# Kernel optimization log

Hardware: AMD Instinct MI355X
Metric: run time of the kernel (lower is better)

Reference implementation:

```python
import jax, jax.numpy as jnp
import numpy as np

DIM = 128        # per-head dim == model width in this module
Q_HEADS = 16
KV_HEADS = 4
WINDOW = 512
BATCH = 4
SEQ = 2048


def setup_inputs() -> dict:
    key = jax.random.key(0)
    k1, k2, k3 = jax.random.split(key, 3)
    x = jax.random.normal(k1, (BATCH, SEQ, DIM), dtype=jnp.float32)
    # fused qkv weight, stored (in, out) so forward is x @ W_qkv
    W_qkv = jax.random.normal(k2, (DIM, (Q_HEADS + 2 * KV_HEADS) * DIM), dtype=jnp.float32) * (DIM ** -0.5)
    W_proj = jax.random.normal(k3, (Q_HEADS * DIM, DIM), dtype=jnp.float32) * ((Q_HEADS * DIM) ** -0.5)
    return {"x": x, "W_qkv": W_qkv, "W_proj": W_proj}


def _gqa_forward(x, W_qkv, W_proj):
    b, s, d = x.shape
    qkv = x @ W_qkv                                    # [b, s, (Hq+2Hkv)*d]
    qkv = qkv.reshape(b, s, Q_HEADS + 2 * KV_HEADS, d).transpose(0, 2, 1, 3)
    q = qkv[:, :Q_HEADS]                               # [b, Hq, s, d]
    k = qkv[:, Q_HEADS:Q_HEADS + KV_HEADS]             # [b, Hkv, s, d]
    v = qkv[:, Q_HEADS + KV_HEADS:]                    # [b, Hkv, s, d]

    # GQA: repeat kv heads to match q heads
    group = Q_HEADS // KV_HEADS
    k = jnp.repeat(k, group, axis=1)                   # [b, Hq, s, d]
    v = jnp.repeat(v, group, axis=1)

    scale = 1.0 / jnp.sqrt(jnp.float32(d))
    scores = jnp.einsum('bhqd,bhkd->bhqk', q, k) * scale   # [b, Hq, s, s]

    q_idx = jnp.arange(s)[:, None]
    kv_idx = jnp.arange(s)[None, :]
    rel = (q_idx - kv_idx).astype(jnp.float32)         # [s, s]
    # per-head ALiBi slope: exp2(-(h+1)*8/Hq), added (sign matches source)
    h = jnp.arange(Q_HEADS, dtype=jnp.float32)
    slopes = jnp.exp2(-((h + 1.0) * 8.0 / Q_HEADS))    # [Hq]
    scores = scores + slopes[None, :, None, None] * rel[None, None, :, :]

    mask = (q_idx >= kv_idx) & ((q_idx - kv_idx) <= WINDOW)
    scores = jnp.where(mask[None, None], scores, -jnp.inf)
    probs = jax.nn.softmax(scores, axis=-1)

    att = jnp.einsum('bhqk,bhkd->bhqd', probs, v)      # [b, Hq, s, d]
    att = att.transpose(0, 2, 1, 3).reshape(b, s, Q_HEADS * d)
    return att @ W_proj                                # [b, s, d]


def reference(x, W_qkv, W_proj):
    return _gqa_forward(x, W_qkv, W_proj)
```

## Files before the change

### kernel.cpp

```cpp
#include <hip/hip_runtime.h>
#include <math.h>

#define DIM_    128
#define QH_     16
#define KVH_    4
#define WIN_    512
#define BATCH_  4
#define SEQ_    2048
#define QKV_LD  3072

#define QB_LD   3136
#define VG_LD   2112
#define AH_LD   2112
#define WP_LD   2112

#define NX   (BATCH_*SEQ_*DIM_)
#define NWQ  (DIM_*QKV_LD)

typedef __attribute__((ext_vector_type(8))) short short8;
typedef __attribute__((ext_vector_type(4))) float f32x4;
typedef unsigned short u16;
typedef unsigned int u32;

__device__ __forceinline__ u16 f2bf(float f) {
    u32 u = __float_as_uint(f);
    u += 0x7fff + ((u >> 16) & 1);
    return (u16)(u >> 16);
}
__device__ __forceinline__ float bf2f(u16 u) {
    return __uint_as_float(((u32)u) << 16);
}
__device__ __forceinline__ u32 pkbf(float a, float b) {
    u32 r;
    __asm__("v_cvt_pk_bf16_f32 %0, %1, %2" : "=v"(r) : "v"(a), "v"(b));
    return r;
}
#define MFMA16 __builtin_amdgcn_mfma_f32_16x16x32_bf16

#if __has_builtin(__builtin_amdgcn_exp2f)
#define EXP2F __builtin_amdgcn_exp2f
#else
#define EXP2F exp2f
#endif

__device__ __forceinline__ void gload_lds16(const u16* g, u16* l) {
    __builtin_amdgcn_global_load_lds(
        (const __attribute__((address_space(1))) unsigned int*)(const void*)g,
        (__attribute__((address_space(3))) unsigned int*)(void*)l, 16, 0, 0);
}

__global__ __launch_bounds__(256) void prep(
    const float* __restrict__ x, const float* __restrict__ Wqkv,
    const float* __restrict__ Wproj,
    u16* __restrict__ xh, u16* __restrict__ wth, u16* __restrict__ wpth)
{
    if (blockIdx.x < 1024) {
        const size_t t = (size_t)blockIdx.x * 256 + threadIdx.x;
        float4 v = *(const float4*)(x + 4 * t);
        ushort4 o;
        o.x = f2bf(v.x); o.y = f2bf(v.y); o.z = f2bf(v.z); o.w = f2bf(v.w);
        *(ushort4*)(xh + 4 * t) = o;
        return;
    }
    __shared__ float T[32][33];
    int tile = blockIdx.x - 1024;
    const float* src; u16* dst; int N, ldo;
    if (tile < 384) { src = Wqkv;  dst = wth;  N = 3072; ldo = 128; }
    else { tile -= 384; src = Wproj; dst = wpth; N = 128; ldo = WP_LD; }
    const int ntile = N >> 5;
    const int k0 = (tile / ntile) << 5, n0 = (tile % ntile) << 5;
    const int tx = threadIdx.x & 31, ty = threadIdx.x >> 5;
    #pragma unroll
    for (int i = 0; i < 4; ++i)
        T[ty + 8 * i][tx] = src[(size_t)(k0 + ty + 8 * i) * N + n0 + tx];
    __syncthreads();
    #pragma unroll
    for (int i = 0; i < 4; ++i)
        dst[(size_t)(n0 + ty + 8 * i) * ldo + k0 + tx] = f2bf(T[tx][ty + 8 * i]);
}

__global__ __launch_bounds__(256) void gemm1_mfma(
    const u16* __restrict__ xh, const u16* __restrict__ wth,
    u16* __restrict__ qkvb, u16* __restrict__ vg)
{
    const int bn = blockIdx.x * 64;
    const int mc = blockIdx.y * 512;
    const int wv = threadIdx.x >> 6, lane = threadIdx.x & 63;
    const int lo = lane & 15, hi = lane >> 4;
    const int lr = lo, quad = hi;

    short8 bf[4][4];
    #pragma unroll
    for (int nt = 0; nt < 4; ++nt)
        #pragma unroll
        for (int s = 0; s < 4; ++s)
            bf[nt][s] = *(const short8*)(
                wth + (size_t)(bn + nt * 16 + lo) * DIM_ + s * 32 + hi * 8);

    const bool qk = (bn < 2560);
    const u16* aA = xh + (size_t)(mc + wv * 16 + lo) * DIM_ + hi * 8;

#define G1BODY(AF, IT) do {                                                   \
    f32x4 acc[4] = {};                                                        \
    if (qk) {                                                                 \
        _Pragma("unroll")                                                     \
        for (int s = 0; s < 4; ++s)                                           \
            _Pragma("unroll")                                                 \
            for (int nt = 0; nt < 4; ++nt)                                    \
                acc[nt] = MFMA16(bf[nt][s], AF[s], acc[nt], 0, 0, 0);         \
        const int row = mc + (IT) * 64 + wv * 16 + lr;                        \
        u16* dst = qkvb + (size_t)row * QB_LD + bn + quad * 4;                \
        _Pragma("unroll")                                                     \
        for (int nt = 0; nt < 4; ++nt) {                                      \
            uint2 o;                                                          \
            o.x = pkbf(acc[nt][0], acc[nt][1]);                               \
            o.y = pkbf(acc[nt][2], acc[nt][3]);                               \
            *(uint2*)(dst + nt * 16) = o;                                     \
        }                                                                     \
    } else {                                                                  \
        _Pragma("unroll")                                                     \
        for (int s = 0; s < 4; ++s)                                           \
            _Pragma("unroll")                                                 \
            for (int nt = 0; nt < 4; ++nt)                                    \
                acc[nt] = MFMA16(AF[s], bf[nt][s], acc[nt], 0, 0, 0);         \
        const int m0 = mc + (IT) * 64 + wv * 16 + quad * 4;                   \
        const int bb = m0 >> 11, mseq = m0 & 2047;                            \
        _Pragma("unroll")                                                     \
        for (int nt = 0; nt < 4; ++nt) {                                      \
            const int ncol = bn + nt * 16 + lr - 2560;                        \
            const int kvh = ncol >> 7, d = ncol & 127;                        \
            uint2 o;                                                          \
            o.x = pkbf(acc[nt][0], acc[nt][1]);                               \
            o.y = pkbf(acc[nt][2], acc[nt][3]);                               \
            *(uint2*)(vg + ((size_t)(bb * KVH_ + kvh) * DIM_ + d) * VG_LD     \
                      + mseq) = o;                                            \
        }                                                                     \
    }                                                                         \
} while (0)

    short8 afA[4], afB[4];
    #pragma unroll
    for (int s = 0; s < 4; ++s) afA[s] = *(const short8*)(aA + s * 32);

    #pragma unroll 1
    for (int it = 0; it < 8; it += 2) {
        const u16* aN = aA + (size_t)(it + 1) * 64 * DIM_;
        #pragma unroll
        for (int s = 0; s < 4; ++s) afB[s] = *(const short8*)(aN + s * 32);
        G1BODY(afA, it);
        const int nx = (it + 2 < 8) ? (it + 2) : 7;
        const u16* aN2 = aA + (size_t)nx * 64 * DIM_;
        #pragma unroll
        for (int s = 0; s < 4; ++s) afA[s] = *(const short8*)(aN2 + s * 32);
        G1BODY(afB, it + 1);
    }
#undef G1BODY
}

__global__ __launch_bounds__(512) void attn_mfma(
    const u16* __restrict__ qkvb, const u16* __restrict__ vg,
    u16* __restrict__ ah, int qoff)
{
    const int xcd  = blockIdx.x & 7;
    const int idx  = blockIdx.x >> 3;
    const int pair = xcd + 8 * (idx & 1);
    const int qt   = (idx >> 1) + qoff;
    const int b    = pair >> 2, kvh = pair & 3;
    const int q0 = qt << 5;
    const int tid = threadIdx.x;
    const int wv8 = tid >> 6, lane = tid & 63;
    const int hq = wv8 >> 1, mrow = wv8 & 1;
    const int lr = lane & 15, quad = lane >> 4;
    const int h = kvh * 4 + hq;
    const bool oddq = (quad & 1) != 0;

    __shared__ u16 Kb[3][8][512];
    __shared__ u16 Vb[3][8][512];

    const float scale2 = 0.08838834764831845f * 1.4426950408889634f;
    const float slope2 = exp2f(-0.5f * (float)(h + 1)) * 1.4426950408889634f;
    const int jbase = max(0, q0 - WIN_);
    const int nch = (q0 + 32 - jbase) >> 5;
    const size_t rowb = (size_t)b * SEQ_;
    const u16* kg  = qkvb + rowb * QB_LD + (QH_ + kvh) * DIM_;
    const u16* vgb = vg + (size_t)(b * KVH_ + kvh) * DIM_ * VG_LD;
    const int lo = lane & 15, hi = lane >> 4;

    short8 qf[4];
    {
        const u16* qp = qkvb + (rowb + q0 + mrow * 16 + lr) * QB_LD
                        + h * DIM_ + quad * 8;
        #pragma unroll
        for (int s = 0; s < 4; ++s) qf[s] = *(const short8*)(qp + 32 * s);
    }

    float alpha0;
    {
        const int q = q0 + mrow * 16 + lr;
        const int rm = (q < WIN_) ? q : WIN_;
        alpha0 = slope2 * (float)(q - rm);
    }

    f32x4 O[8] = {};
    float rs = 0.f;

    #define STAGE(CH, SLOT) do {                                              \
        const int _jk = jbase + ((CH) << 5);                                  \
        gload_lds16(kg + (size_t)(_jk + (wv8 >> 2) * 16 + lo) * QB_LD         \
                    + (wv8 & 3) * 32 + hi * 8, &Kb[(SLOT)][wv8][0]);          \
        gload_lds16(vgb + (size_t)(wv8 * 16 + lo) * VG_LD + _jk + hi * 8,     \
                    &Vb[(SLOT)][wv8][0]);                                     \
    } while (0)

    STAGE(0, 0);
    STAGE(1, 1);

    for (int ch = 0; ch < nch; ++ch) {
        const int jk = jbase + (ch << 5);
        const int slot = ch % 3;
        __asm__ volatile("s_waitcnt vmcnt(2)" ::: "memory");
        __asm__ volatile("s_barrier" ::: "memory");
        { const int cn = (ch + 2 < nch) ? (ch + 2) : (nch - 1);
          STAGE(cn, (ch + 2) % 3); }

        u32 pw[2][2];
        const int qm0 = q0 + mrow * 16;
        #pragma unroll
        for (int nt = 0; nt < 2; ++nt) {
            f32x4 c = {0.f, 0.f, 0.f, 0.f};
            __builtin_amdgcn_s_setprio(1);
            #pragma unroll
            for (int s = 0; s < 4; ++s) {
                short8 kf = *(const short8*)&Kb[slot][nt * 4 + s][lane * 8];
                c = MFMA16(kf, qf[s], c, 0, 0, 0);
            }
            __builtin_amdgcn_s_setprio(0);
            const int jknt = jk + nt * 16;
            const float b0 = fmaf(-slope2, (float)(jknt + quad * 4), alpha0);
            float e0, e1, e2, e3;
            if (qm0 >= jknt + 15 && qm0 + 15 <= jknt + WIN_) {
                e0 = EXP2F(fmaf(c[0], scale2, b0));
                e1 = EXP2F(fmaf(c[1], scale2, b0 - slope2));
                e2 = EXP2F(fmaf(c[2], scale2, b0 - 2.f * slope2));
                e3 = EXP2F(fmaf(c[3], scale2, b0 - 3.f * slope2));
            } else {
                const int q = qm0 + lr, j0q = jknt + quad * 4;
                float ee[4];
                #pragma unroll
                for (int r = 0; r < 4; ++r) {
                    const int rel = q - (j0q + r);
                    const float t = fmaf(c[r], scale2, b0 - (float)r * slope2);
                    ee[r] = ((unsigned)rel <= (unsigned)WIN_) ? EXP2F(t) : 0.f;
                }
                e0 = ee[0]; e1 = ee[1]; e2 = ee[2]; e3 = ee[3];
            }
            rs += (e0 + e1) + (e2 + e3);
            pw[nt][0] = pkbf(e0, e1);
            pw[nt][1] = pkbf(e2, e3);
        }

        short8 pa;
        {
            union { u32 w[4]; short8 s; } P;
            #pragma unroll
            for (int w = 0; w < 2; ++w) {
                auto r = __builtin_amdgcn_permlane32_swap(
                    pw[0][w], pw[1][w], false, false);
                const u32 rx = r[0], ry = r[1];
                const u32 sx = (u32)__shfl_xor((int)rx, 16);
                const u32 sy = (u32)__shfl_xor((int)ry, 16);
                P.w[w]     = oddq ? sy : rx;
                P.w[2 + w] = oddq ? ry : sx;
            }
            pa = P.s;
        }

        __builtin_amdgcn_s_setprio(1);
        #pragma unroll
        for (int nt = 0; nt < 8; ++nt) {
            short8 vf = *(const short8*)&Vb[slot][nt][lane * 8];
            O[nt] = MFMA16(vf, pa, O[nt], 0, 0, 0);
        }
        __builtin_amdgcn_s_setprio(0);
    }
    #undef STAGE

    __asm__ volatile("s_waitcnt vmcnt(0)" ::: "memory");

    rs += __shfl_xor(rs, 16);
    rs += __shfl_xor(rs, 32);

    {
        const float inv = 1.0f / rs;
        u16* dst = ah + (rowb + q0 + mrow * 16 + lr) * (size_t)AH_LD
                   + h * DIM_;
        #pragma unroll
        for (int nt = 0; nt < 8; ++nt) {
            uint2 o;
            o.x = pkbf(O[nt][0] * inv, O[nt][1] * inv);
            o.y = pkbf(O[nt][2] * inv, O[nt][3] * inv);
            *(uint2*)(dst + nt * 16 + quad * 4) = o;
        }
    }
}

__global__ __launch_bounds__(512) void gemm2_mfma(
    const u16* __restrict__ ah, const u16* __restrict__ wpth,
    float* __restrict__ out)
{
    const int bm = blockIdx.x * 64;
    const int tid = threadIdx.x;
    const int wv8 = tid >> 6, lane = tid & 63;
    const int wr = wv8 >> 2, wc = wv8 & 3;
    const int lr = lane & 15, quad = lane >> 4;
    const int lo = lr, hi = quad;

    __shared__ u16 At[3][8][512];
    __shared__ u16 Wt[3][16][512];

    #define G2STAGE(CH, SLOT) do {                                            \
        const int _jk = (CH) << 6;                                            \
        {   const int _mt = wv8 >> 1, _s = wv8 & 1;        \
            gload_lds16(ah + (size_t)(bm + _mt * 16 + lo) * AH_LD             \
                        + _jk + _s * 32 + hi * 8, &At[(SLOT)][wv8][0]); }     \
        _Pragma("unroll")                                                     \
        for (int _t = 0; _t < 2; ++_t) {               \
            const int _p = wv8 + _t * 8;                                      \
            const int _nt = _p >> 1, _s = _p & 1;                             \
            gload_lds16(wpth + (size_t)(_nt * 16 + lo) * WP_LD                \
                        + _jk + _s * 32 + hi * 8, &Wt[(SLOT)][_p][0]);        \
        }                                                                     \
    } while (0)

    f32x4 acc[2][2] = {};

    G2STAGE(0, 0);
    G2STAGE(1, 1);

    for (int ch = 0; ch < 32; ++ch) {
        const int slot = ch % 3;
        __asm__ volatile("s_waitcnt vmcnt(3)" ::: "memory");
        __asm__ volatile("s_barrier" ::: "memory");
        { const int cn = (ch + 2 < 32) ? (ch + 2) : 31;
          G2STAGE(cn, (ch + 2) % 3); }

        #pragma unroll
        for (int s = 0; s < 2; ++s) {
            short8 af[2], wf[2];
            #pragma unroll
            for (int mt = 0; mt < 2; ++mt)
                af[mt] = *(const short8*)&At[slot][(wr * 2 + mt) * 2 + s][lane * 8];
            #pragma unroll
            for (int nt = 0; nt < 2; ++nt)
                wf[nt] = *(const short8*)&Wt[slot][(wc * 2 + nt) * 2 + s][lane * 8];
            __builtin_amdgcn_s_setprio(1);
            #pragma unroll
            for (int mt = 0; mt < 2; ++mt)
                #pragma unroll
                for (int nt = 0; nt < 2; ++nt)
                    acc[mt][nt] = MFMA16(wf[nt], af[mt], acc[mt][nt], 0, 0, 0);
            __builtin_amdgcn_s_setprio(0);
        }
    }
    #undef G2STAGE

    __asm__ volatile("s_waitcnt vmcnt(0)" ::: "memory");

    #pragma unroll
    for (int mt = 0; mt < 2; ++mt)
        #pragma unroll
        for (int nt = 0; nt < 2; ++nt) {
            float* orow = out + (size_t)(bm + (wr * 2 + mt) * 16 + lr) * DIM_
                          + (wc * 2 + nt) * 16 + quad * 4;
            *(float4*)orow = *(float4*)&acc[mt][nt];
        }
}

extern "C" void kernel_launch(void* const* d_in, const int* in_sizes, int n_in,
                              void* d_out, int out_size, void* d_ws, size_t ws_size,
                              hipStream_t stream)
{
    const float* x     = (const float*)d_in[0];
    const float* Wqkv  = (const float*)d_in[1];
    const float* Wproj = (const float*)d_in[2];
    float* out = (float*)d_out;

    u16* xh   = (u16*)d_ws;
    u16* wth  = xh   + (size_t)NX;
    u16* wpth = wth  + (size_t)NWQ;
    u16* qkvb = wpth + (size_t)DIM_ * WP_LD;
    u16* vg   = qkvb + (size_t)8192 * QB_LD;
    u16* ahp  = vg   + (size_t)BATCH_ * KVH_ * DIM_ * VG_LD;

    prep<<<1024 + 640, 256, 0, stream>>>(x, Wqkv, Wproj, xh, wth, wpth);

    gemm1_mfma<<<dim3(48, 16), 256, 0, stream>>>(xh, wth, qkvb, vg);

    attn_mfma<<<512, 512, 0, stream>>>(qkvb, vg, ahp, 0);
    attn_mfma<<<512, 512, 0, stream>>>(qkvb, vg, ahp, 32);

    gemm2_mfma<<<8192 / 64, 512, 0, stream>>>(ahp, wpth, out);
}
```

Baseline: 199.4 us.

## Restructure output-projection GEMM: smaller M tile, direct W loads, coarse K stages

The output projection GEMM now uses 32-row M tiles, which doubles the block count to 256 so more CUs are busy. Only the activation tile is staged through LDS, in four 512-wide K chunks with double buffering. The weight fragments are read straight from global memory through the cache and no longer go through LDS. This removes the 32-step fine-grained pipeline and its barriers, but each wave now issues more global weight loads and loses the LDS sharing of W across waves.

```diff
diff --git a/kernel.cpp b/kernel.cpp
--- a/kernel.cpp
+++ b/kernel.cpp
@@ -308,58 +308,44 @@
     const u16* __restrict__ ah, const u16* __restrict__ wpth,
     float* __restrict__ out)
 {
-    const int bm = blockIdx.x * 64;
+    const int bm = blockIdx.x * 32;
     const int tid = threadIdx.x;
     const int wv8 = tid >> 6, lane = tid & 63;
     const int wr = wv8 >> 2, wc = wv8 & 3;
     const int lr = lane & 15, quad = lane >> 4;
-    const int lo = lr, hi = quad;
-
-    __shared__ u16 At[3][8][512];
-    __shared__ u16 Wt[3][16][512];
-
-    #define G2STAGE(CH, SLOT) do {                                            \
-        const int _jk = (CH) << 6;                                            \
-        {   const int _mt = wv8 >> 1, _s = wv8 & 1;        \
-            gload_lds16(ah + (size_t)(bm + _mt * 16 + lo) * AH_LD             \
-                        + _jk + _s * 32 + hi * 8, &At[(SLOT)][wv8][0]); }     \
-        _Pragma("unroll")                                                     \
-        for (int _t = 0; _t < 2; ++_t) {               \
-            const int _p = wv8 + _t * 8;                                      \
-            const int _nt = _p >> 1, _s = _p & 1;                             \
-            gload_lds16(wpth + (size_t)(_nt * 16 + lo) * WP_LD                \
-                        + _jk + _s * 32 + hi * 8, &Wt[(SLOT)][_p][0]);        \
+
+    __shared__ u16 At2[2][32][520];
+
+    #define G2STAGE(KS, SLOT) do {                                            \
+        _Pragma("unroll")                                                     \
+        for (int _t = 0; _t < 4; ++_t) {                                      \
+            const int _r = wv8 * 4 + _t;                                      \
+            gload_lds16(ah + (size_t)(bm + _r) * AH_LD + (KS) * 512           \
+                        + lane * 8, &At2[(SLOT)][_r][0]);                     \
         }                                                                     \
     } while (0)
 
-    f32x4 acc[2][2] = {};
+    f32x4 acc[2] = {};
 
     G2STAGE(0, 0);
-    G2STAGE(1, 1);
-
-    for (int ch = 0; ch < 32; ++ch) {
-        const int slot = ch % 3;
-        __asm__ volatile("s_waitcnt vmcnt(3)" ::: "memory");
+
+    #pragma unroll 1
+    for (int ks = 0; ks < 4; ++ks) {
+        const int slot = ks & 1;
+        __asm__ volatile("s_waitcnt vmcnt(0)" ::: "memory");
         __asm__ volatile("s_barrier" ::: "memory");
-        { const int cn = (ch + 2 < 32) ? (ch + 2) : 31;
-          G2STAGE(cn, (ch + 2) % 3); }
-
-        #pragma unroll
-        for (int s = 0; s < 2; ++s) {
-            short8 af[2], wf[2];
-            #pragma unroll
-            for (int mt = 0; mt < 2; ++mt)
-                af[mt] = *(const short8*)&At[slot][(wr * 2 + mt) * 2 + s][lane * 8];
-            #pragma unroll
-            for (int nt = 0; nt < 2; ++nt)
-                wf[nt] = *(const short8*)&Wt[slot][(wc * 2 + nt) * 2 + s][lane * 8];
-            __builtin_amdgcn_s_setprio(1);
-            #pragma unroll
-            for (int mt = 0; mt < 2; ++mt)
-                #pragma unroll
-                for (int nt = 0; nt < 2; ++nt)
-                    acc[mt][nt] = MFMA16(wf[nt], af[mt], acc[mt][nt], 0, 0, 0);
-            __builtin_amdgcn_s_setprio(0);
+        if (ks < 3) G2STAGE(ks + 1, slot ^ 1);
+
+        const u16* wbase = wpth + (size_t)(wc * 32 + lr) * WP_LD
+                           + ks * 512 + quad * 8;
+        #pragma unroll
+        for (int s = 0; s < 16; ++s) {
+            short8 wf0 = *(const short8*)(wbase + s * 32);
+            short8 wf1 = *(const short8*)(wbase + (size_t)16 * WP_LD + s * 32);
+            short8 af  = *(const short8*)
+                &At2[slot][wr * 16 + lr][s * 32 + quad * 8];
+            acc[0] = MFMA16(wf0, af, acc[0], 0, 0, 0);
+            acc[1] = MFMA16(wf1, af, acc[1], 0, 0, 0);
         }
     }
     #undef G2STAGE
@@ -367,13 +353,11 @@
     __asm__ volatile("s_waitcnt vmcnt(0)" ::: "memory");
 
     #pragma unroll
-    for (int mt = 0; mt < 2; ++mt)
-        #pragma unroll
-        for (int nt = 0; nt < 2; ++nt) {
-            float* orow = out + (size_t)(bm + (wr * 2 + mt) * 16 + lr) * DIM_
-                          + (wc * 2 + nt) * 16 + quad * 4;
-            *(float4*)orow = *(float4*)&acc[mt][nt];
-        }
+    for (int nt = 0; nt < 2; ++nt) {
+        float* orow = out + (size_t)(bm + wr * 16 + lr) * DIM_
+                      + wc * 32 + nt * 16 + quad * 4;
+        *(float4*)orow = *(float4*)&acc[nt];
+    }
 }
 
 extern "C" void kernel_launch(void* const* d_in, const int* in_sizes, int n_in,
@@ -399,5 +383,5 @@
     attn_mfma<<<512, 512, 0, stream>>>(qkvb, vg, ahp, 0);
     attn_mfma<<<512, 512, 0, stream>>>(qkvb, vg, ahp, 32);
 
-    gemm2_mfma<<<8192 / 64, 512, 0, stream>>>(ahp, wpth, out);
-}
+    gemm2_mfma<<<8192 / 32, 512, 0, stream>>>(ahp, wpth, out);
+}
```

After: 191.6 us. 3.9% less time.
